# Kernel tuning notes

Measured on AMD Instinct MI355X. Metric: run time of the kernel, lower is better.

Reference implementation:

```python
import jax, jax.numpy as jnp
import numpy as np

B, D, K = 65536, 128, 8
BOUND = 3.0
MIN_BIN_W = 1e-3   # min_bin_width
MIN_BIN_H = 1e-3   # min_bin_height
MIN_DERIV = 1e-3   # min_derivative
EPS = 1e-6


def setup_inputs() -> dict:
    key = jax.random.key(0)
    k1, k2, k3, k4 = jax.random.split(key, 4)
    return {
        "x": jax.random.normal(k1, (B, D), jnp.float32) * 1.5,
        "unnormalized_widths": jax.random.normal(k2, (D, K), jnp.float32),
        "unnormalized_heights": jax.random.normal(k3, (D, K), jnp.float32),
        "unnormalized_derivatives": jax.random.normal(k4, (D, K - 1), jnp.float32),
    }


def _calculate_knots(lengths, lower, upper):
    # lengths: [D, K] summing to ~1 -> scaled lengths and knot positions [D, K+1]
    knots = jnp.cumsum(lengths, axis=-1)
    knots = jnp.pad(knots, ((0, 0), (1, 0)))
    knots = (upper - lower) * knots + lower
    knots = knots.at[..., 0].set(lower)
    knots = knots.at[..., -1].set(upper)
    return knots[..., 1:] - knots[..., :-1], knots


def _select_bins(p, idx):
    # p: [D, Kp] per-dim tables, idx: [B, D] bin indices -> [B, D]
    i = jnp.clip(idx, 0, p.shape[-1] - 1)
    return p[jnp.arange(p.shape[0])[None, :], i]


def _spline_forward(x, uw, uh, ud):
    w = jax.nn.softmax(uw, axis=-1)
    h = jax.nn.softmax(uh, axis=-1)
    d = jax.nn.softplus(ud)

    num_bins = w.shape[-1]
    widths = MIN_BIN_W + (1.0 - MIN_BIN_W * num_bins) * w
    heights = MIN_BIN_H + (1.0 - MIN_BIN_H * num_bins) * h
    derivs = jnp.pad(MIN_DERIV + d, ((0, 0), (1, 1)), constant_values=1.0 - MIN_DERIV)  # [D, K+1]

    widths, cumwidths = _calculate_knots(widths, -BOUND, BOUND)
    heights, cumheights = _calculate_knots(heights, -BOUND, BOUND)

    inside = (x >= -BOUND) & (x <= BOUND)
    xc = jnp.clip(x, -BOUND, BOUND)  # keep tail values finite; masked out below

    # searchsorted: which bin each input falls into   [B, D]
    bin_idx = jnp.sum(xc[..., None] >= (cumwidths + EPS)[None, :, :], axis=-1) - 1

    iw = _select_bins(widths, bin_idx)
    icw = _select_bins(cumwidths, bin_idx)
    ich = _select_bins(cumheights, bin_idx)
    idelta = _select_bins(heights / widths, bin_idx)
    id0 = _select_bins(derivs, bin_idx)
    id1 = _select_bins(derivs[..., 1:], bin_idx)
    ih = _select_bins(heights, bin_idx)

    # rational quadratic spline (forward)
    theta = (xc - icw) / iw
    t1m = theta * (1.0 - theta)
    numerator = ih * (idelta * theta ** 2 + id0 * t1m)
    denominator = idelta + (id0 + id1 - 2.0 * idelta) * t1m
    out = ich + numerator / denominator
    dnum = idelta ** 2 * (id1 * theta ** 2 + 2.0 * idelta * t1m + id0 * (1.0 - theta) ** 2)
    lad = jnp.log(dnum) - 2.0 * jnp.log(denominator)

    u = jnp.where(inside, out, x)          # identity outside tail bound
    lad = jnp.where(inside, lad, 0.0)
    return u, lad


def reference(x, unnormalized_widths, unnormalized_heights, unnormalized_derivatives):
    u, lad = _spline_forward(x, unnormalized_widths, unnormalized_heights, unnormalized_derivatives)
    log_detJ = jnp.sum(lad, axis=1)
    return u, log_detJ
```

## Files before the change

### kernel.cpp

```cpp
#include <hip/hip_runtime.h>
#include <math.h>

namespace {
constexpr int D = 128;
constexpr int K = 8;
constexpr float BOUND = 3.0f;
constexpr float EPS = 1e-6f;
constexpr float MIN_BIN_W = 1e-3f;
constexpr float MIN_BIN_H = 1e-3f;
constexpr float MIN_DERIV = 1e-3f;
constexpr int REC = 8;
constexpr int S = K * REC + 4;
constexpr int WPB = 4;
}

__device__ __forceinline__ float spline_one(float xv, const float* __restrict__ row,
                                            const float* kn, float* __restrict__ outp) {
    const bool inside = (xv >= -BOUND) & (xv <= BOUND);
    const float xc = fminf(fmaxf(xv, -BOUND), BOUND);
    int idx = 0;
    #pragma unroll
    for (int j = 0; j < 7; ++j) idx += (xc >= kn[j]) ? 1 : 0;
    const float4 ra = *(const float4*)(row + idx * REC);
    const float4 rb = *(const float4*)(row + idx * REC + 4);
    const float theta = (xc - ra.x) * ra.y;
    const float omt   = 1.f - theta;
    const float t1m   = theta * omt;
    const float th2   = theta * theta;
    const float num   = rb.y * (ra.w * th2 + ra.z * t1m);
    const float den   = ra.w + rb.w * t1m;
    const float outv  = rb.x + __fdividef(num, den);
    const float dnum  = ra.w * ra.w * (rb.z * th2 + 2.f * ra.w * t1m + ra.z * omt * omt);
    const float lad   = __logf(dnum) - 2.f * __logf(den);
    *outp = inside ? outv : xv;
    return inside ? lad : 0.f;
}

__global__ __launch_bounds__(256) void spline_fwd(
    const float* __restrict__ x,
    const float* __restrict__ uw,
    const float* __restrict__ uh,
    const float* __restrict__ ud,
    float* __restrict__ out_u,
    float* __restrict__ out_ld,
    int nrows)
{
    __shared__ __align__(16) float s_tab[D * S];

    const int tid = threadIdx.x;
    if (tid < D) {
        const int d = tid;
        float wv[K], hv[K], cw[K + 1], ch[K + 1], der[K + 1];

        {
            const float* p = uw + d * K;
            float m = p[0];
            #pragma unroll
            for (int j = 1; j < K; ++j) m = fmaxf(m, p[j]);
            float s = 0.f;
            #pragma unroll
            for (int j = 0; j < K; ++j) { wv[j] = __expf(p[j] - m); s += wv[j]; }
            const float inv = 1.f / s;
            #pragma unroll
            for (int j = 0; j < K; ++j)
                wv[j] = MIN_BIN_W + (1.f - MIN_BIN_W * K) * (wv[j] * inv);
        }
        {
            const float* p = uh + d * K;
            float m = p[0];
            #pragma unroll
            for (int j = 1; j < K; ++j) m = fmaxf(m, p[j]);
            float s = 0.f;
            #pragma unroll
            for (int j = 0; j < K; ++j) { hv[j] = __expf(p[j] - m); s += hv[j]; }
            const float inv = 1.f / s;
            #pragma unroll
            for (int j = 0; j < K; ++j)
                hv[j] = MIN_BIN_H + (1.f - MIN_BIN_H * K) * (hv[j] * inv);
        }
        cw[0] = -BOUND; ch[0] = -BOUND;
        float cs_w = 0.f, cs_h = 0.f;
        #pragma unroll
        for (int j = 0; j < K; ++j) {
            cs_w += wv[j]; cw[j + 1] = 2.f * BOUND * cs_w - BOUND;
            cs_h += hv[j]; ch[j + 1] = 2.f * BOUND * cs_h - BOUND;
        }
        cw[K] = BOUND; ch[K] = BOUND;

        der[0] = 1.f - MIN_DERIV;
        der[K] = 1.f - MIN_DERIV;
        {
            const float* p = ud + d * (K - 1);
            #pragma unroll
            for (int j = 1; j < K; ++j) {
                const float v = p[j - 1];
                const float sp = log1pf(__expf(-fabsf(v))) + fmaxf(v, 0.f);
                der[j] = MIN_DERIV + sp;
            }
        }

        float* row = s_tab + d * S;
        #pragma unroll
        for (int j = 0; j < K; ++j) {
            const float w  = cw[j + 1] - cw[j];
            const float h  = ch[j + 1] - ch[j];
            const float dl = h / w;
            row[j * REC + 0] = cw[j];
            row[j * REC + 1] = 1.f / w;
            row[j * REC + 2] = der[j];
            row[j * REC + 3] = dl;
            row[j * REC + 4] = ch[j];
            row[j * REC + 5] = h;
            row[j * REC + 6] = der[j + 1];
            row[j * REC + 7] = der[j] + der[j + 1] - 2.f * dl;
        }
    }
    __syncthreads();

    const int wave = tid >> 6;
    const int lane = tid & 63;
    const int da = lane;
    const int db = lane + 64;
    const float* rowa = s_tab + da * S;
    const float* rowb = s_tab + db * S;

    float kna[7], knb[7];
    #pragma unroll
    for (int j = 0; j < 7; ++j) {
        kna[j] = rowa[(j + 1) * REC] + EPS;
        knb[j] = rowb[(j + 1) * REC] + EPS;
    }

    const int rstep = gridDim.x * WPB;
    for (int r = blockIdx.x * WPB + wave; r < nrows; r += rstep) {
        const float* xr = x + (size_t)r * D;
        float* ur = out_u + (size_t)r * D;
        const float xa = xr[da];
        const float xb = xr[db];
        float lacc = spline_one(xa, rowa, kna, ur + da)
                   + spline_one(xb, rowb, knb, ur + db);
        #pragma unroll
        for (int off = 32; off > 0; off >>= 1)
            lacc += __shfl_down(lacc, off);
        if (lane == 0) out_ld[r] = lacc;
    }
}

extern "C" void kernel_launch(void* const* d_in, const int* in_sizes, int n_in,
                              void* d_out, int out_size, void* d_ws, size_t ws_size,
                              hipStream_t stream) {
    const float* x  = (const float*)d_in[0];
    const float* uw = (const float*)d_in[1];
    const float* uh = (const float*)d_in[2];
    const float* ud = (const float*)d_in[3];
    const int nrows = in_sizes[0] / D;
    float* out_u  = (float*)d_out;
    float* out_ld = (float*)d_out + (size_t)nrows * D;
    spline_fwd<<<1024, 256, 0, stream>>>(x, uw, uh, ud, out_u, out_ld, nrows);
}
```

Measured before the change: 103.2 us.

## Vectorize row processing with float4 loads, four dims per lane, and two-row batching

Each lane now handles four consecutive dimensions through float4 loads and stores, and each wave processes two pairs of rows per iteration. Half-wave shuffle reductions replace the full-wave reduction. The division is replaced by a hardware reciprocal, and the two logs are folded into a single log of dnum*rd*rd. A minimum-blocks-per-SM hint of 4 is added to the launch bounds. Together these aim to cut memory instruction count and transcendental work, at the cost of more registers (28 knots per lane) and a slightly different rounding in the log-determinant.

```diff
diff --git a/kernel.cpp b/kernel.cpp
--- a/kernel.cpp
+++ b/kernel.cpp
@@ -14,8 +14,8 @@
 constexpr int WPB = 4;
 }
 
-__device__ __forceinline__ float spline_one(float xv, const float* __restrict__ row,
-                                            const float* kn, float* __restrict__ outp) {
+__device__ __forceinline__ float spline_elem(float xv, const float* __restrict__ row,
+                                             const float* kn, float* __restrict__ outp) {
     const bool inside = (xv >= -BOUND) & (xv <= BOUND);
     const float xc = fminf(fmaxf(xv, -BOUND), BOUND);
     int idx = 0;
@@ -29,14 +29,15 @@
     const float th2   = theta * theta;
     const float num   = rb.y * (ra.w * th2 + ra.z * t1m);
     const float den   = ra.w + rb.w * t1m;
-    const float outv  = rb.x + __fdividef(num, den);
+    const float rd    = __builtin_amdgcn_rcpf(den);
+    const float outv  = fmaf(num, rd, rb.x);
     const float dnum  = ra.w * ra.w * (rb.z * th2 + 2.f * ra.w * t1m + ra.z * omt * omt);
-    const float lad   = __logf(dnum) - 2.f * __logf(den);
+    const float lad   = __logf(dnum * rd * rd);
     *outp = inside ? outv : xv;
     return inside ? lad : 0.f;
 }
 
-__global__ __launch_bounds__(256) void spline_fwd(
+__global__ __launch_bounds__(256, 4) void spline_fwd(
     const float* __restrict__ x,
     const float* __restrict__ uw,
     const float* __restrict__ uh,
@@ -119,30 +120,60 @@
 
     const int wave = tid >> 6;
     const int lane = tid & 63;
-    const int da = lane;
-    const int db = lane + 64;
-    const float* rowa = s_tab + da * S;
-    const float* rowb = s_tab + db * S;
+    const int l32  = lane & 31;
+    const int half = lane >> 5;
+    const int dbase = l32 << 2;
 
-    float kna[7], knb[7];
+    const float* rowp0 = s_tab + (dbase + 0) * S;
+    const float* rowp1 = s_tab + (dbase + 1) * S;
+    const float* rowp2 = s_tab + (dbase + 2) * S;
+    const float* rowp3 = s_tab + (dbase + 3) * S;
+
+    float kn[28];
     #pragma unroll
     for (int j = 0; j < 7; ++j) {
-        kna[j] = rowa[(j + 1) * REC] + EPS;
-        knb[j] = rowb[(j + 1) * REC] + EPS;
+        kn[j]      = rowp0[(j + 1) * REC] + EPS;
+        kn[7 + j]  = rowp1[(j + 1) * REC] + EPS;
+        kn[14 + j] = rowp2[(j + 1) * REC] + EPS;
+        kn[21 + j] = rowp3[(j + 1) * REC] + EPS;
     }
 
-    const int rstep = gridDim.x * WPB;
-    for (int r = blockIdx.x * WPB + wave; r < nrows; r += rstep) {
-        const float* xr = x + (size_t)r * D;
-        float* ur = out_u + (size_t)r * D;
-        const float xa = xr[da];
-        const float xb = xr[db];
-        float lacc = spline_one(xa, rowa, kna, ur + da)
-                   + spline_one(xb, rowb, knb, ur + db);
-        #pragma unroll
-        for (int off = 32; off > 0; off >>= 1)
-            lacc += __shfl_down(lacc, off);
-        if (lane == 0) out_ld[r] = lacc;
+    const int npairs = nrows >> 1;
+    const int gw = blockIdx.x * WPB + wave;
+    const int nw = gridDim.x * WPB;
+    const int lo4 = lane << 2;
+
+    for (int p = gw * 2; p < npairs; p += nw * 2) {
+        const int r0 = p * 2;
+        const float4 xa = *(const float4*)(x + (size_t)r0 * D + lo4);
+        const bool two = (p + 1) < npairs;
+        const int r2 = two ? (p + 1) * 2 : r0;
+        const float4 xb = *(const float4*)(x + (size_t)r2 * D + lo4);
+
+        float4 ua, ub;
+        float la, lb;
+        la  = spline_elem(xa.x, rowp0, kn +  0, &ua.x);
+        la += spline_elem(xa.y, rowp1, kn +  7, &ua.y);
+        la += spline_elem(xa.z, rowp2, kn + 14, &ua.z);
+        la += spline_elem(xa.w, rowp3, kn + 21, &ua.w);
+        lb  = spline_elem(xb.x, rowp0, kn +  0, &ub.x);
+        lb += spline_elem(xb.y, rowp1, kn +  7, &ub.y);
+        lb += spline_elem(xb.z, rowp2, kn + 14, &ub.z);
+        lb += spline_elem(xb.w, rowp3, kn + 21, &ub.w);
+
+        *(float4*)(out_u + (size_t)r0 * D + lo4) = ua;
+        if (two) *(float4*)(out_u + (size_t)r2 * D + lo4) = ub;
+
+        la += __shfl_xor(la, 1);  lb += __shfl_xor(lb, 1);
+        la += __shfl_xor(la, 2);  lb += __shfl_xor(lb, 2);
+        la += __shfl_xor(la, 4);  lb += __shfl_xor(lb, 4);
+        la += __shfl_xor(la, 8);  lb += __shfl_xor(lb, 8);
+        la += __shfl_xor(la, 16); lb += __shfl_xor(lb, 16);
+
+        if (l32 == 0) {
+            out_ld[r0 + half] = la;
+            if (two) out_ld[r2 + half] = lb;
+        }
     }
 }
 
```

Result: no change. 104.5 us (+1.3%).

## Vectorize row I/O with float4 per lane, batch rows per wave, fuse logs

Applied to the files above, without the earlier changes.

Each wave now handles pairs of rows, and every lane loads and stores a float4 of four consecutive dims, so global traffic uses 128-bit accesses. Each wave prefetches PPW row pairs up front to raise memory-level parallelism. The shared table is laid out in four interleaved groups so the four dims per lane come from separate 32-row blocks. The two logs collapse into a single log2 of dnum/den² scaled by ln2, and the division becomes a reciprocal plus FMA. The grid is sized to the problem, which makes many more blocks that each rebuild the per-dim table, and the kernel assumes an even row count.

```diff
diff --git a/kernel.cpp b/kernel.cpp
--- a/kernel.cpp
+++ b/kernel.cpp
@@ -9,13 +9,15 @@
 constexpr float MIN_BIN_W = 1e-3f;
 constexpr float MIN_BIN_H = 1e-3f;
 constexpr float MIN_DERIV = 1e-3f;
+constexpr float LN2 = 0.6931471805599453f;
 constexpr int REC = 8;
 constexpr int S = K * REC + 4;
 constexpr int WPB = 4;
+constexpr int PPW = 4;
 }
 
-__device__ __forceinline__ float spline_one(float xv, const float* __restrict__ row,
-                                            const float* kn, float* __restrict__ outp) {
+__device__ __forceinline__ float spline_elem(float xv, const float* __restrict__ row,
+                                             const float* kn, float* __restrict__ outp) {
     const bool inside = (xv >= -BOUND) & (xv <= BOUND);
     const float xc = fminf(fmaxf(xv, -BOUND), BOUND);
     int idx = 0;
@@ -29,9 +31,10 @@
     const float th2   = theta * theta;
     const float num   = rb.y * (ra.w * th2 + ra.z * t1m);
     const float den   = ra.w + rb.w * t1m;
-    const float outv  = rb.x + __fdividef(num, den);
+    const float rd    = __builtin_amdgcn_rcpf(den);
+    const float outv  = fmaf(num, rd, rb.x);
     const float dnum  = ra.w * ra.w * (rb.z * th2 + 2.f * ra.w * t1m + ra.z * omt * omt);
-    const float lad   = __logf(dnum) - 2.f * __logf(den);
+    const float lad   = __log2f(dnum * rd * rd);
     *outp = inside ? outv : xv;
     return inside ? lad : 0.f;
 }
@@ -99,7 +102,7 @@
             }
         }
 
-        float* row = s_tab + d * S;
+        float* row = s_tab + ((d & 3) * 32 + (d >> 2)) * S;
         #pragma unroll
         for (int j = 0; j < K; ++j) {
             const float w  = cw[j + 1] - cw[j];
@@ -119,30 +122,55 @@
 
     const int wave = tid >> 6;
     const int lane = tid & 63;
-    const int da = lane;
-    const int db = lane + 64;
-    const float* rowa = s_tab + da * S;
-    const float* rowb = s_tab + db * S;
+    const int l32  = lane & 31;
+    const int half = lane >> 5;
 
-    float kna[7], knb[7];
+    const float* rowp0 = s_tab + (0 * 32 + l32) * S;
+    const float* rowp1 = s_tab + (1 * 32 + l32) * S;
+    const float* rowp2 = s_tab + (2 * 32 + l32) * S;
+    const float* rowp3 = s_tab + (3 * 32 + l32) * S;
+
+    float kn[28];
     #pragma unroll
     for (int j = 0; j < 7; ++j) {
-        kna[j] = rowa[(j + 1) * REC] + EPS;
-        knb[j] = rowb[(j + 1) * REC] + EPS;
+        kn[j]      = rowp0[(j + 1) * REC] + EPS;
+        kn[7 + j]  = rowp1[(j + 1) * REC] + EPS;
+        kn[14 + j] = rowp2[(j + 1) * REC] + EPS;
+        kn[21 + j] = rowp3[(j + 1) * REC] + EPS;
     }
 
-    const int rstep = gridDim.x * WPB;
-    for (int r = blockIdx.x * WPB + wave; r < nrows; r += rstep) {
-        const float* xr = x + (size_t)r * D;
-        float* ur = out_u + (size_t)r * D;
-        const float xa = xr[da];
-        const float xb = xr[db];
-        float lacc = spline_one(xa, rowa, kna, ur + da)
-                   + spline_one(xb, rowb, knb, ur + db);
-        #pragma unroll
-        for (int off = 32; off > 0; off >>= 1)
-            lacc += __shfl_down(lacc, off);
-        if (lane == 0) out_ld[r] = lacc;
+    const int npairs = nrows >> 1;
+    const int p0 = (blockIdx.x * WPB + wave) * PPW;
+    const int lo4 = lane << 2;
+
+    float4 xv[PPW];
+    #pragma unroll
+    for (int c = 0; c < PPW; ++c) {
+        const int p = p0 + c;
+        const int pc = (p < npairs) ? p : (npairs - 1);
+        xv[c] = *(const float4*)(x + (size_t)(pc * 2) * D + lo4);
+    }
+
+    #pragma unroll
+    for (int c = 0; c < PPW; ++c) {
+        const int p = p0 + c;
+        if (p < npairs) {
+            float4 u;
+            float la;
+            la  = spline_elem(xv[c].x, rowp0, kn +  0, &u.x);
+            la += spline_elem(xv[c].y, rowp1, kn +  7, &u.y);
+            la += spline_elem(xv[c].z, rowp2, kn + 14, &u.z);
+            la += spline_elem(xv[c].w, rowp3, kn + 21, &u.w);
+
+            *(float4*)(out_u + (size_t)(p * 2) * D + lo4) = u;
+
+            la += __shfl_xor(la, 1);
+            la += __shfl_xor(la, 2);
+            la += __shfl_xor(la, 4);
+            la += __shfl_xor(la, 8);
+            la += __shfl_xor(la, 16);
+            if (l32 == 0) out_ld[p * 2 + half] = la * LN2;
+        }
     }
 }
 
@@ -156,5 +184,8 @@
     const int nrows = in_sizes[0] / D;
     float* out_u  = (float*)d_out;
     float* out_ld = (float*)d_out + (size_t)nrows * D;
-    spline_fwd<<<1024, 256, 0, stream>>>(x, uw, uh, ud, out_u, out_ld, nrows);
+    const int npairs = nrows / 2;
+    const int nwaves = (npairs + PPW - 1) / PPW;
+    const int nblocks = (nwaves + WPB - 1) / WPB;
+    spline_fwd<<<nblocks, 256, 0, stream>>>(x, uw, uh, ud, out_u, out_ld, nrows);
 }
```

Measured after the change: 102.7 us. Within noise of the previous version (-0.4%).
